# Kernel tuning notes

Hardware: AMD Instinct MI355X
Metric: run time of the kernel (lower is better)

Reference implementation:

```python
import jax, jax.numpy as jnp
import numpy as np
from jax import lax

N = 16384       # input points
STRIDE = 4
M = N // STRIDE # sampled centers (single batch: n_o = [o[0]//stride])
NSAMPLE = 16
CIN = 64
COUT = 128
EPS = 1e-5      # BatchNorm1d default eps


def setup_inputs() -> dict:
    key = jax.random.key(0)
    k1, k2, k3, k4 = jax.random.split(key, 4)
    p = jax.random.normal(k1, (N, 3), dtype=jnp.float32)
    n = jax.random.normal(k2, (N, 3), dtype=jnp.float32)
    x = jax.random.normal(k3, (N, CIN), dtype=jnp.float32)
    o = jnp.array([N], dtype=jnp.int32)  # single point cloud
    W = jax.random.normal(k4, (COUT, 3 + CIN), dtype=jnp.float32) * 0.05
    gamma = jnp.ones((COUT,), dtype=jnp.float32)
    beta = jnp.zeros((COUT,), dtype=jnp.float32)
    return {"p": p, "n": n, "x": x, "o": o, "W": W, "gamma": gamma, "beta": beta}


def _fps(p, m):
    """Furthest point sampling (pointops.furthestsampling), single batch."""
    npts = p.shape[0]
    def step(carry, _):
        dists, last = carry
        d = jnp.sum((p - p[last]) ** 2, axis=-1)
        dists = jnp.minimum(dists, d)
        nxt = jnp.argmax(dists).astype(jnp.int32)
        return (dists, nxt), nxt
    first = jnp.int32(0)
    init = (jnp.full((npts,), 1e10, dtype=p.dtype), first)
    _, rest = lax.scan(step, init, None, length=m - 1)
    return jnp.concatenate([first[None], rest])  # [m]


def reference(p, n, x, o, W, gamma, beta):
    # --- furthest sampling: n_o = [o[0]//stride] = [M] (static for single batch)
    idx = _fps(p, M)                      # [M] int32
    n_p = p[idx]                          # [M,3] new coords
    n_n = n[idx]                          # [M,3] new normals
    # --- queryandgroup: kNN of each center in full cloud, use_xyz=True
    d2 = (jnp.sum(n_p * n_p, -1)[:, None]
          + jnp.sum(p * p, -1)[None, :]
          - 2.0 * n_p @ p.T)              # [M,N]
    _, knn = lax.top_k(-lax.stop_gradient(d2), NSAMPLE)   # [M,NSAMPLE]
    grouped_xyz = p[knn] - n_p[:, None, :]                # [M,NS,3] relative coords
    grouped_x = x[knn]                                    # [M,NS,CIN]
    feat = jnp.concatenate([grouped_xyz, grouped_x], axis=-1)  # [M,NS,3+CIN]
    # --- linear (no bias) -> BN (training stats, per channel) -> ReLU -> max over neighbors
    y = jnp.einsum('msc,oc->mso', feat, W)                # [M,NS,COUT]
    mean = jnp.mean(y, axis=(0, 1))
    var = jnp.mean((y - mean) ** 2, axis=(0, 1))          # biased var (torch BN)
    y = (y - mean) * lax.rsqrt(var + EPS) * gamma + beta
    y = jax.nn.relu(y)
    y = jnp.max(y, axis=1)                                # MaxPool1d(nsample) -> [M,COUT]
    n_o = jnp.array([M], dtype=jnp.int32)
    return (n_p, n_n, y, n_o)
```

## Files before the change

kernel.cpp:

```cpp
#include <hip/hip_runtime.h>
#include <math.h>

#define N_PTS 16384
#define M_CTR 4096
#define NS 16
#define CIN 64
#define COUT 128
#define CFEAT 67
#define CPB 4
#define NCELL 512

__device__ __forceinline__ unsigned ordu(float f) {
    unsigned b = __float_as_uint(f);
    return (b & 0x80000000u) ? ~b : (b | 0x80000000u);
}
__device__ __forceinline__ float unord(unsigned u) {
    unsigned b = (u & 0x80000000u) ? (u & 0x7FFFFFFFu) : ~u;
    return __uint_as_float(b);
}

__device__ __forceinline__ void pmerge(unsigned long long& a1, unsigned long long& a2,
                                       unsigned long long b1, unsigned long long b2) {
    unsigned long long n1 = a1 > b1 ? a1 : b1;
    unsigned long long lo = a1 > b1 ? b1 : a1;
    unsigned long long m2 = a2 > b2 ? a2 : b2;
    a2 = lo > m2 ? lo : m2;
    a1 = n1;
}

#define DPP_TOP2(CTRL) do { \
    unsigned _o1lo = (unsigned)__builtin_amdgcn_update_dpp(0, (int)(unsigned)k1, CTRL, 0xF, 0xF, false); \
    unsigned _o1hi = (unsigned)__builtin_amdgcn_update_dpp(0, (int)(unsigned)(k1>>32), CTRL, 0xF, 0xF, false); \
    unsigned _o2lo = (unsigned)__builtin_amdgcn_update_dpp(0, (int)(unsigned)k2, CTRL, 0xF, 0xF, false); \
    unsigned _o2hi = (unsigned)__builtin_amdgcn_update_dpp(0, (int)(unsigned)(k2>>32), CTRL, 0xF, 0xF, false); \
    unsigned long long _b1 = ((unsigned long long)_o1hi << 32) | (unsigned long long)_o1lo; \
    unsigned long long _b2 = ((unsigned long long)_o2hi << 32) | (unsigned long long)_o2lo; \
    pmerge(k1, k2, _b1, _b2); \
} while (0)

#define DPP_SWEEP(M) M(0x111); M(0x112); M(0x114); M(0x118); M(0x142); M(0x143)

__global__ void init_kernel(unsigned* __restrict__ bmin, unsigned* __restrict__ bmax,
                            int* __restrict__ cnt, int* __restrict__ fill)
{
    int i = blockIdx.x * blockDim.x + threadIdx.x;
    if (i < NCELL * 3) { bmin[i] = 0xFFFFFFFFu; bmax[i] = 0u; }
    if (i < NCELL) { cnt[i] = 0; fill[i] = 0; }
}

__global__ __launch_bounds__(256) void bbox_kernel(const float* __restrict__ p,
                                                   float* __restrict__ gbb)
{
    int t = threadIdx.x, lane = t & 63, w = t >> 6;
    float mnx = 1e30f, mny = 1e30f, mnz = 1e30f;
    float mxx = -1e30f, mxy = -1e30f, mxz = -1e30f;
    for (int i = t; i < N_PTS; i += 256) {
        float x = p[i*3], y = p[i*3+1], z = p[i*3+2];
        mnx = fminf(mnx, x); mny = fminf(mny, y); mnz = fminf(mnz, z);
        mxx = fmaxf(mxx, x); mxy = fmaxf(mxy, y); mxz = fmaxf(mxz, z);
    }
    for (int m = 1; m < 64; m <<= 1) {
        mnx = fminf(mnx, __shfl_xor(mnx, m)); mny = fminf(mny, __shfl_xor(mny, m));
        mnz = fminf(mnz, __shfl_xor(mnz, m));
        mxx = fmaxf(mxx, __shfl_xor(mxx, m)); mxy = fmaxf(mxy, __shfl_xor(mxy, m));
        mxz = fmaxf(mxz, __shfl_xor(mxz, m));
    }
    __shared__ float s[4][6];
    if (lane == 0) { s[w][0]=mnx; s[w][1]=mny; s[w][2]=mnz; s[w][3]=mxx; s[w][4]=mxy; s[w][5]=mxz; }
    __syncthreads();
    if (t == 0) {
        gbb[0] = fminf(fminf(s[0][0], s[1][0]), fminf(s[2][0], s[3][0]));
        gbb[1] = fminf(fminf(s[0][1], s[1][1]), fminf(s[2][1], s[3][1]));
        gbb[2] = fminf(fminf(s[0][2], s[1][2]), fminf(s[2][2], s[3][2]));
        gbb[3] = fmaxf(fmaxf(s[0][3], s[1][3]), fmaxf(s[2][3], s[3][3]));
        gbb[4] = fmaxf(fmaxf(s[0][4], s[1][4]), fmaxf(s[2][4], s[3][4]));
        gbb[5] = fmaxf(fmaxf(s[0][5], s[1][5]), fmaxf(s[2][5], s[3][5]));
    }
}

__global__ void assign_kernel(const float* __restrict__ p, const float* __restrict__ gbb,
                              int* __restrict__ c_of, int* __restrict__ cnt)
{
    int i = blockIdx.x * blockDim.x + threadIdx.x;
    if (i >= N_PTS) return;
    float bx = gbb[0], by = gbb[1], bz = gbb[2];
    float sx = 7.9999f / fmaxf(gbb[3] - bx, 1e-20f);
    float sy = 7.9999f / fmaxf(gbb[4] - by, 1e-20f);
    float sz = 7.9999f / fmaxf(gbb[5] - bz, 1e-20f);
    float x = p[i*3], y = p[i*3+1], z = p[i*3+2];
    int ix = min(7, max(0, (int)((x - bx) * sx)));
    int iy = min(7, max(0, (int)((y - by) * sy)));
    int iz = min(7, max(0, (int)((z - bz) * sz)));
    int c = (ix << 6) | (iy << 3) | iz;
    c_of[i] = c;
    atomicAdd(&cnt[c], 1);
}

__global__ __launch_bounds__(512) void prefix_kernel(const int* __restrict__ cnt,
                                                     int* __restrict__ start,
                                                     int* __restrict__ cmeta)
{
    __shared__ int a[NCELL];
    int t = threadIdx.x;
    int v = cnt[t]; a[t] = v; __syncthreads();
    for (int off = 1; off < NCELL; off <<= 1) {
        int u = (t >= off) ? a[t - off] : 0;
        __syncthreads();
        a[t] += u;
        __syncthreads();
    }
    int st = a[t] - v;
    start[t] = st;
    cmeta[t] = (st << 15) | v;
}

__global__ void scatter_kernel(const float* __restrict__ p, const int* __restrict__ c_of,
                               const int* __restrict__ start, int* __restrict__ fill,
                               float4* __restrict__ sp, unsigned* __restrict__ bmin,
                               unsigned* __restrict__ bmax)
{
    int i = blockIdx.x * blockDim.x + threadIdx.x;
    if (i >= N_PTS) return;
    int c = c_of[i];
    int pos = start[c] + atomicAdd(&fill[c], 1);
    float x = p[i*3], y = p[i*3+1], z = p[i*3+2];
    sp[pos] = make_float4(x, y, z, __int_as_float(i));
    atomicMin(&bmin[c*3+0], ordu(x)); atomicMax(&bmax[c*3+0], ordu(x));
    atomicMin(&bmin[c*3+1], ordu(y)); atomicMax(&bmax[c*3+1], ordu(y));
    atomicMin(&bmin[c*3+2], ordu(z)); atomicMax(&bmax[c*3+2], ordu(z));
}

__global__ __launch_bounds__(1024) void fps_kernel(const float* __restrict__ p,
                                                   const float4* __restrict__ sp,
                                                   const int* __restrict__ g_cmeta,
                                                   const unsigned* __restrict__ g_bmin,
                                                   const unsigned* __restrict__ g_bmax,
                                                   int* __restrict__ sel)
{
    __shared__ float distl[N_PTS];
    __shared__ unsigned long long key1[NCELL], key2[NCELL];
    __shared__ int cmeta_s[NCELL];
    __shared__ unsigned short wl[NCELL];
    __shared__ float bq[6];
    __shared__ int bnsel;
    __shared__ int wlc;

    const int t = threadIdx.x;
    const int lane = t & 63, wave = t >> 6;

    for (int i = t; i < N_PTS; i += 1024) distl[i] = 1e10f;

    int my_cnt = 0;
    float mnx=0.f, mny=0.f, mnz=0.f, mxx=0.f, mxy=0.f, mxz=0.f;
    if (t < NCELL) {
        int meta = g_cmeta[t];
        cmeta_s[t] = meta;
        my_cnt = meta & 0x7FFF;
        mnx = unord(g_bmin[t*3+0]); mny = unord(g_bmin[t*3+1]); mnz = unord(g_bmin[t*3+2]);
        mxx = unord(g_bmax[t*3+0]); mxy = unord(g_bmax[t*3+1]); mxz = unord(g_bmax[t*3+2]);
        key1[t] = 0ull; key2[t] = 0ull;
    }
    if (t == 0) { wlc = 0; sel[0] = 0; }
    float q1x = p[0], q1y = p[1], q1z = p[2];
    float q2x = 0.f, q2y = 0.f, q2z = 0.f;
    bool two = false;
    bool first = true;
    __syncthreads();

    int it = 1;
    while (it < M_CTR) {
        bool act = false;
        if (my_cnt > 0) {
            if (first) act = true;
            else {
                float cm = __uint_as_float((unsigned)(key1[t] >> 32)) * 1.00001f;
                float ddx = fmaxf(fmaxf(__fsub_rn(mnx, q1x), __fsub_rn(q1x, mxx)), 0.f);
                float ddy = fmaxf(fmaxf(__fsub_rn(mny, q1y), __fsub_rn(q1y, mxy)), 0.f);
                float ddz = fmaxf(fmaxf(__fsub_rn(mnz, q1z), __fsub_rn(q1z, mxz)), 0.f);
                float dm1 = __fadd_rn(__fadd_rn(__fmul_rn(ddx,ddx), __fmul_rn(ddy,ddy)),
                                      __fmul_rn(ddz,ddz));
                act = dm1 < cm;
                if (!act && two) {
                    float ex = fmaxf(fmaxf(__fsub_rn(mnx, q2x), __fsub_rn(q2x, mxx)), 0.f);
                    float ey = fmaxf(fmaxf(__fsub_rn(mny, q2y), __fsub_rn(q2y, mxy)), 0.f);
                    float ez = fmaxf(fmaxf(__fsub_rn(mnz, q2z), __fsub_rn(q2z, mxz)), 0.f);
                    float dm2 = __fadd_rn(__fadd_rn(__fmul_rn(ex,ex), __fmul_rn(ey,ey)),
                                          __fmul_rn(ez,ez));
                    act = dm2 < cm;
                }
            }
        }
        unsigned long long mask = __ballot(act);
        int base = 0;
        if (lane == 0 && mask) base = atomicAdd(&wlc, (int)__popcll(mask));
        base = __shfl(base, 0);
        if (act)
            wl[base + (int)__popcll(mask & ((1ull << lane) - 1ull))] = (unsigned short)t;
        __syncthreads();
        const int nwl = wlc;

        for (int e = wave; e < nwl; e += 16) {
            int c = wl[e];
            int mv = cmeta_s[c];
            int st = mv >> 15, cnt = mv & 0x7FFF;
            unsigned long long k1 = 0ull, k2 = 0ull;
            for (int o = lane; o < cnt; o += 64) {
                int g = st + o;
                float4 P = sp[g];
                float D = distl[g];
                float dx = __fsub_rn(P.x, q1x), dy = __fsub_rn(P.y, q1y), dz = __fsub_rn(P.z, q1z);
                float d2 = __fadd_rn(__fadd_rn(__fmul_rn(dx,dx), __fmul_rn(dy,dy)),
                                     __fmul_rn(dz,dz));
                float nd = fminf(D, d2);
                if (two) {
                    float ex = __fsub_rn(P.x, q2x), ey = __fsub_rn(P.y, q2y), ez = __fsub_rn(P.z, q2z);
                    float e2 = __fadd_rn(__fadd_rn(__fmul_rn(ex,ex), __fmul_rn(ey,ey)),
                                         __fmul_rn(ez,ez));
                    nd = fminf(nd, e2);
                }
                distl[g] = nd;
                unsigned long long kk = ((unsigned long long)__float_as_uint(nd) << 32)
                                      | (unsigned long long)(~(unsigned)__float_as_int(P.w));
                if (kk > k1) { k2 = k1; k1 = kk; }
                else if (kk > k2) { k2 = kk; }
            }
            DPP_SWEEP(DPP_TOP2);
            if (lane == 63) { key1[c] = k1; key2[c] = k2; }
        }
        if (t == 1023) wlc = 0;
        __syncthreads();

        if (wave == 0) {
            unsigned long long k1 = 0ull, k2 = 0ull;
#pragma unroll
            for (int j = 0; j < 8; ++j) {
                int c = lane + (j << 6);
                pmerge(k1, k2, key1[c], key2[c]);
            }
            DPP_SWEEP(DPP_TOP2);
            if (lane == 63) {
                unsigned long long A1 = k1, A2 = k2;
                int s1 = (int)(~(unsigned)(A1 & 0xFFFFFFFFull));
                int s2 = (int)(~(unsigned)(A2 & 0xFFFFFFFFull));
                sel[it] = s1;
                float nq1x = p[s1*3+0], nq1y = p[s1*3+1], nq1z = p[s1*3+2];
                float bx2 = p[s2*3+0], by2 = p[s2*3+1], bz2 = p[s2*3+2];
                int nsel = 1;
                if (A2 != 0ull && it + 1 < M_CTR) {
                    float dx = __fsub_rn(bx2, nq1x), dy = __fsub_rn(by2, nq1y), dz = __fsub_rn(bz2, nq1z);
                    float d2b = __fadd_rn(__fadd_rn(__fmul_rn(dx,dx), __fmul_rn(dy,dy)),
                                          __fmul_rn(dz,dz));
                    float db = __uint_as_float((unsigned)(A2 >> 32));
                    if (d2b >= db) { nsel = 2; sel[it + 1] = s2; }
                }
                bq[0] = nq1x; bq[1] = nq1y; bq[2] = nq1z;
                bq[3] = bx2;  bq[4] = by2;  bq[5] = bz2;
                bnsel = nsel;
            }
        }
        __syncthreads();
        int nsel = bnsel;
        q1x = bq[0]; q1y = bq[1]; q1z = bq[2];
        two = (nsel == 2);
        if (two) { q2x = bq[3]; q2y = bq[4]; q2z = bq[5]; }
        first = false;
        it += nsel;
    }
}

__global__ void prep_kernel(const float* __restrict__ p, const float* __restrict__ nrm,
                            const int* __restrict__ sel, float* __restrict__ pp2,
                            float* __restrict__ out)
{
    int i = blockIdx.x * blockDim.x + threadIdx.x;
    if (i < N_PTS) {
        float x = p[i*3], y = p[i*3+1], z = p[i*3+2];
        pp2[i] = __fadd_rn(__fadd_rn(__fmul_rn(x,x), __fmul_rn(y,y)), __fmul_rn(z,z));
    }
    if (i < M_CTR) {
        int j = sel[i];
        out[i*3+0] = p[j*3+0]; out[i*3+1] = p[j*3+1]; out[i*3+2] = p[j*3+2];
        out[12288 + i*3+0] = nrm[j*3+0];
        out[12288 + i*3+1] = nrm[j*3+1];
        out[12288 + i*3+2] = nrm[j*3+2];
    }
    if (i == 0) out[548864] = (float)M_CTR;
}

__global__ __launch_bounds__(256) void knn_kernel(const float* __restrict__ p,
                                                  const float* __restrict__ pp2,
                                                  const float* __restrict__ np ,
                                                  int* __restrict__ knn)
{
    const int lane = threadIdx.x & 63;
    const int wave = threadIdx.x >> 6;
    const int c = blockIdx.x * 4 + wave;

    float cx = np[c*3], cy = np[c*3+1], cz = np[c*3+2];
    float c2 = __fadd_rn(__fadd_rn(__fmul_rn(cx,cx), __fmul_rn(cy,cy)), __fmul_rn(cz,cz));

    float hd[16]; int hi[16];
#pragma unroll
    for (int k = 0; k < 16; ++k) { hd[k] = 1e30f; hi[k] = 0x7fffffff; }

    for (int t = 0; t < N_PTS/64; ++t) {
        int j = t*64 + lane;
        float px = p[j*3+0], py = p[j*3+1], pz = p[j*3+2];
        float dot = __fadd_rn(__fadd_rn(__fmul_rn(cx,px), __fmul_rn(cy,py)),
                              __fmul_rn(cz,pz));
        float d2  = __fsub_rn(__fadd_rn(c2, pp2[j]), __fmul_rn(2.0f, dot));
        if (d2 < hd[15]) {
#pragma unroll
            for (int k = 15; k >= 1; --k) {
                bool up   = d2 < hd[k-1];
                bool here = d2 < hd[k];
                hd[k] = up ? hd[k-1] : (here ? d2 : hd[k]);
                hi[k] = up ? hi[k-1] : (here ? j  : hi[k]);
            }
            if (d2 < hd[0]) { hd[0] = d2; hi[0] = j; }
        }
    }

    for (int r = 0; r < 16; ++r) {
        float wv = hd[0]; int wi = hi[0];
#pragma unroll
        for (int m = 1; m < 64; m <<= 1) {
            float ov = __shfl_xor(wv, m);
            int   oi = __shfl_xor(wi, m);
            bool b = (ov < wv) || (ov == wv && oi < wi);
            wv = b ? ov : wv; wi = b ? oi : wi;
        }
        if (hi[0] == wi) {
            knn[c*16 + r] = wi;
#pragma unroll
            for (int k = 0; k < 15; ++k) { hd[k] = hd[k+1]; hi[k] = hi[k+1]; }
            hd[15] = 1e30f; hi[15] = 0x7fffffff;
        }
    }
}

__global__ __launch_bounds__(128) void passA_kernel(const float* __restrict__ p,
                                                    const float* __restrict__ xf,
                                                    const float* __restrict__ W,
                                                    const int* __restrict__ knn,
                                                    const float* __restrict__ out ,
                                                    float* __restrict__ ymax,
                                                    float* __restrict__ ymin,
                                                    float* __restrict__ partials)
{
    __shared__ float Wt[CFEAT][COUT];
    __shared__ float ft[CPB][NS][CFEAT];
    __shared__ float bsum[CPB][COUT], bssq[CPB][COUT];

    const int t = threadIdx.x;
    const int mbase = blockIdx.x * CPB;

    for (int c = 0; c < CFEAT; ++c) Wt[c][t] = W[t*CFEAT + c];

    {
        int r = t >> 1, half = t & 1;
        int ci = r >> 4, s = r & 15;
        int m = mbase + ci;
        int nb = knn[m*NS + s];
        if (half == 0) {
            ft[ci][s][0] = __fsub_rn(p[nb*3+0], out[m*3+0]);
            ft[ci][s][1] = __fsub_rn(p[nb*3+1], out[m*3+1]);
            ft[ci][s][2] = __fsub_rn(p[nb*3+2], out[m*3+2]);
        }
        for (int c = half*32; c < half*32 + 32; ++c)
            ft[ci][s][3+c] = xf[nb*CIN + c];
    }
    __syncthreads();

    const int ci = t >> 5, l = t & 31;
    float acc[NS][4];
#pragma unroll
    for (int s = 0; s < NS; ++s) { acc[s][0]=0.f; acc[s][1]=0.f; acc[s][2]=0.f; acc[s][3]=0.f; }

    for (int c = 0; c < CFEAT; ++c) {
        float w0 = Wt[c][l], w1 = Wt[c][l+32], w2 = Wt[c][l+64], w3 = Wt[c][l+96];
#pragma unroll
        for (int s = 0; s < NS; ++s) {
            float f = ft[ci][s][c];
            acc[s][0] = fmaf(f, w0, acc[s][0]);
            acc[s][1] = fmaf(f, w1, acc[s][1]);
            acc[s][2] = fmaf(f, w2, acc[s][2]);
            acc[s][3] = fmaf(f, w3, acc[s][3]);
        }
    }

    const int m = mbase + ci;
#pragma unroll
    for (int j = 0; j < 4; ++j) {
        int o = l + 32*j;
        float s = 0.f, q = 0.f, mx = -1e30f, mn = 1e30f;
#pragma unroll
        for (int sidx = 0; sidx < NS; ++sidx) {
            float v = acc[sidx][j];
            s += v; q = fmaf(v, v, q);
            mx = fmaxf(mx, v); mn = fminf(mn, v);
        }
        bsum[ci][o] = s;
        bssq[ci][o] = q;
        ymax[m*COUT + o] = mx;
        ymin[m*COUT + o] = mn;
    }
    __syncthreads();
    if (t < COUT) {
        float s = bsum[0][t] + bsum[1][t] + bsum[2][t] + bsum[3][t];
        float q = bssq[0][t] + bssq[1][t] + bssq[2][t] + bssq[3][t];
        partials[t*1024          + blockIdx.x] = s;
        partials[(COUT + t)*1024 + blockIdx.x] = q;
    }
}

__global__ __launch_bounds__(256) void bnstat_kernel(const float* __restrict__ partials,
                                                     const float* __restrict__ gamma,
                                                     const float* __restrict__ beta,
                                                     float* __restrict__ scaleshift)
{
    __shared__ float red[256];
    int t = threadIdx.x;
    const float4* v4 = (const float4*)(partials + t*1024);
    float s = 0.f;
    for (int i = 0; i < 256; ++i) {
        float4 v = v4[i];
        s += v.x; s += v.y; s += v.z; s += v.w;
    }
    red[t] = s;
    __syncthreads();
    if (t < COUT) {
        const float inv = 1.0f / 65536.0f;
        float mean = red[t] * inv;
        float var  = red[COUT + t] * inv - mean*mean;
        float rstd = rsqrtf(var + 1e-5f);
        float g = gamma[t] * rstd;
        scaleshift[t]        = g;
        scaleshift[COUT + t] = beta[t] - mean * g;
    }
}

__global__ void final_kernel(float* __restrict__ y,
                             const float* __restrict__ ymin,
                             const float* __restrict__ scaleshift)
{
    int i = blockIdx.x * blockDim.x + threadIdx.x;
    if (i >= M_CTR * COUT) return;
    int o = i & (COUT - 1);
    float a = scaleshift[o], b = scaleshift[COUT + o];
    float v = (a >= 0.f) ? y[i] : ymin[i];
    float z = fmaf(a, v, b);
    y[i] = fmaxf(z, 0.f);
}

extern "C" void kernel_launch(void* const* d_in, const int* in_sizes, int n_in,
                              void* d_out, int out_size, void* d_ws, size_t ws_size,
                              hipStream_t stream)
{
    const float* p     = (const float*)d_in[0];
    const float* nrm   = (const float*)d_in[1];
    const float* xf    = (const float*)d_in[2];
    const float* W     = (const float*)d_in[4];
    const float* gamma = (const float*)d_in[5];
    const float* beta  = (const float*)d_in[6];

    float* out = (float*)d_out;
    char* ws = (char*)d_ws;
    int*   sel        = (int*)(ws + 0);
    float* pp2        = (float*)(ws + 16384);
    int*   knn        = (int*)(ws + 81920);
    float* ymin       = (float*)(ws + 344064);
    float* partials   = (float*)(ws + 2441216);
    float* scaleshift = (float*)(ws + 3489792);

    float4*   sp        = (float4*)(ws + 81920);
    char*     yb        = ws + 344064;
    int*      c_of      = (int*)(yb + 65536);
    int*      cellcnt   = (int*)(yb + 131072);
    int*      cellfill  = (int*)(yb + 133120);
    int*      cellstart = (int*)(yb + 135168);
    unsigned* bbmin_u   = (unsigned*)(yb + 137216);
    unsigned* bbmax_u   = (unsigned*)(yb + 143360);
    float*    gbb       = (float*)(yb + 149504);
    int*      cmeta_g   = (int*)(yb + 149536);

    float* ymax = out + 24576;

    init_kernel   <<<8,  256, 0, stream>>>(bbmin_u, bbmax_u, cellcnt, cellfill);
    bbox_kernel   <<<1,  256, 0, stream>>>(p, gbb);
    assign_kernel <<<64, 256, 0, stream>>>(p, gbb, c_of, cellcnt);
    prefix_kernel <<<1,  512, 0, stream>>>(cellcnt, cellstart, cmeta_g);
    scatter_kernel<<<64, 256, 0, stream>>>(p, c_of, cellstart, cellfill, sp, bbmin_u, bbmax_u);
    fps_kernel    <<<1,  1024, 0, stream>>>(p, sp, cmeta_g, bbmin_u, bbmax_u, sel);
    prep_kernel   <<<64, 256, 0, stream>>>(p, nrm, sel, pp2, out);
    knn_kernel    <<<1024, 256, 0, stream>>>(p, pp2, out, knn);
    passA_kernel  <<<M_CTR/CPB, 128, 0, stream>>>(p, xf, W, knn, out, ymax, ymin, partials);
    bnstat_kernel <<<1, 256, 0, stream>>>(partials, gamma, beta, scaleshift);
    final_kernel  <<<2048, 256, 0, stream>>>(ymax, ymin, scaleshift);
}
```

Baseline: 6.438 ms.

## Keep FPS distances in registers with fixed 16-point per-thread chunks

New measurement: 6.698 ms. 1.04x slower.

```diff
diff --git a/kernel.cpp b/kernel.cpp
--- a/kernel.cpp
+++ b/kernel.cpp
@@ -8,16 +8,8 @@
 #define COUT 128
 #define CFEAT 67
 #define CPB 4
-#define NCELL 512
-
-__device__ __forceinline__ unsigned ordu(float f) {
-    unsigned b = __float_as_uint(f);
-    return (b & 0x80000000u) ? ~b : (b | 0x80000000u);
-}
-__device__ __forceinline__ float unord(unsigned u) {
-    unsigned b = (u & 0x80000000u) ? (u & 0x7FFFFFFFu) : ~u;
-    return __uint_as_float(b);
-}
+#define NCELL 4096
+#define PPT 16
 
 __device__ __forceinline__ void pmerge(unsigned long long& a1, unsigned long long& a2,
                                        unsigned long long b1, unsigned long long b2) {
@@ -40,11 +32,12 @@
 
 #define DPP_SWEEP(M) M(0x111); M(0x112); M(0x114); M(0x118); M(0x142); M(0x143)
 
-__global__ void init_kernel(unsigned* __restrict__ bmin, unsigned* __restrict__ bmax,
-                            int* __restrict__ cnt, int* __restrict__ fill)
+#define REPEAT16(M) M(0) M(1) M(2) M(3) M(4) M(5) M(6) M(7) \
+                    M(8) M(9) M(10) M(11) M(12) M(13) M(14) M(15)
+
+__global__ void init_kernel(int* __restrict__ cnt, int* __restrict__ fill)
 {
     int i = blockIdx.x * blockDim.x + threadIdx.x;
-    if (i < NCELL * 3) { bmin[i] = 0xFFFFFFFFu; bmax[i] = 0u; }
     if (i < NCELL) { cnt[i] = 0; fill[i] = 0; }
 }
 
@@ -84,159 +77,139 @@
     int i = blockIdx.x * blockDim.x + threadIdx.x;
     if (i >= N_PTS) return;
     float bx = gbb[0], by = gbb[1], bz = gbb[2];
-    float sx = 7.9999f / fmaxf(gbb[3] - bx, 1e-20f);
-    float sy = 7.9999f / fmaxf(gbb[4] - by, 1e-20f);
-    float sz = 7.9999f / fmaxf(gbb[5] - bz, 1e-20f);
+    float sx = 15.9999f / fmaxf(gbb[3] - bx, 1e-20f);
+    float sy = 15.9999f / fmaxf(gbb[4] - by, 1e-20f);
+    float sz = 15.9999f / fmaxf(gbb[5] - bz, 1e-20f);
     float x = p[i*3], y = p[i*3+1], z = p[i*3+2];
-    int ix = min(7, max(0, (int)((x - bx) * sx)));
-    int iy = min(7, max(0, (int)((y - by) * sy)));
-    int iz = min(7, max(0, (int)((z - bz) * sz)));
-    int c = (ix << 6) | (iy << 3) | iz;
+    int ix = min(15, max(0, (int)((x - bx) * sx)));
+    int iy = min(15, max(0, (int)((y - by) * sy)));
+    int iz = min(15, max(0, (int)((z - bz) * sz)));
+    int c = (ix << 8) | (iy << 4) | iz;
     c_of[i] = c;
     atomicAdd(&cnt[c], 1);
 }
 
-__global__ __launch_bounds__(512) void prefix_kernel(const int* __restrict__ cnt,
-                                                     int* __restrict__ start,
-                                                     int* __restrict__ cmeta)
-{
-    __shared__ int a[NCELL];
+__global__ __launch_bounds__(1024) void prefix_kernel(const int* __restrict__ cnt,
+                                                      int* __restrict__ start)
+{
+    __shared__ int a[1024];
     int t = threadIdx.x;
-    int v = cnt[t]; a[t] = v; __syncthreads();
-    for (int off = 1; off < NCELL; off <<= 1) {
+    int c0 = cnt[4*t], c1 = cnt[4*t+1], c2 = cnt[4*t+2], c3 = cnt[4*t+3];
+    int s = c0 + c1 + c2 + c3;
+    a[t] = s; __syncthreads();
+    for (int off = 1; off < 1024; off <<= 1) {
         int u = (t >= off) ? a[t - off] : 0;
         __syncthreads();
         a[t] += u;
         __syncthreads();
     }
-    int st = a[t] - v;
-    start[t] = st;
-    cmeta[t] = (st << 15) | v;
+    int ex = a[t] - s;
+    start[4*t]   = ex;
+    start[4*t+1] = ex + c0;
+    start[4*t+2] = ex + c0 + c1;
+    start[4*t+3] = ex + c0 + c1 + c2;
 }
 
 __global__ void scatter_kernel(const float* __restrict__ p, const int* __restrict__ c_of,
                                const int* __restrict__ start, int* __restrict__ fill,
-                               float4* __restrict__ sp, unsigned* __restrict__ bmin,
-                               unsigned* __restrict__ bmax)
+                               float4* __restrict__ sp)
 {
     int i = blockIdx.x * blockDim.x + threadIdx.x;
     if (i >= N_PTS) return;
     int c = c_of[i];
     int pos = start[c] + atomicAdd(&fill[c], 1);
-    float x = p[i*3], y = p[i*3+1], z = p[i*3+2];
-    sp[pos] = make_float4(x, y, z, __int_as_float(i));
-    atomicMin(&bmin[c*3+0], ordu(x)); atomicMax(&bmax[c*3+0], ordu(x));
-    atomicMin(&bmin[c*3+1], ordu(y)); atomicMax(&bmax[c*3+1], ordu(y));
-    atomicMin(&bmin[c*3+2], ordu(z)); atomicMax(&bmax[c*3+2], ordu(z));
+    sp[pos] = make_float4(p[i*3], p[i*3+1], p[i*3+2], __int_as_float(i));
 }
 
 __global__ __launch_bounds__(1024) void fps_kernel(const float* __restrict__ p,
                                                    const float4* __restrict__ sp,
-                                                   const int* __restrict__ g_cmeta,
-                                                   const unsigned* __restrict__ g_bmin,
-                                                   const unsigned* __restrict__ g_bmax,
                                                    int* __restrict__ sel)
 {
-    __shared__ float distl[N_PTS];
-    __shared__ unsigned long long key1[NCELL], key2[NCELL];
-    __shared__ int cmeta_s[NCELL];
-    __shared__ unsigned short wl[NCELL];
+    __shared__ unsigned long long skw1[16], skw2[16];
     __shared__ float bq[6];
     __shared__ int bnsel;
-    __shared__ int wlc;
 
     const int t = threadIdx.x;
     const int lane = t & 63, wave = t >> 6;
-
-    for (int i = t; i < N_PTS; i += 1024) distl[i] = 1e10f;
-
-    int my_cnt = 0;
-    float mnx=0.f, mny=0.f, mnz=0.f, mxx=0.f, mxy=0.f, mxz=0.f;
-    if (t < NCELL) {
-        int meta = g_cmeta[t];
-        cmeta_s[t] = meta;
-        my_cnt = meta & 0x7FFF;
-        mnx = unord(g_bmin[t*3+0]); mny = unord(g_bmin[t*3+1]); mnz = unord(g_bmin[t*3+2]);
-        mxx = unord(g_bmax[t*3+0]); mxy = unord(g_bmax[t*3+1]); mxz = unord(g_bmax[t*3+2]);
-        key1[t] = 0ull; key2[t] = 0ull;
-    }
-    if (t == 0) { wlc = 0; sel[0] = 0; }
+    const int base = t << 4;
+
+#define DECL(k) float ds##k = 1e10f;
+    REPEAT16(DECL)
+#undef DECL
+
+    float bmnx = 1e30f, bmny = 1e30f, bmnz = 1e30f;
+    float bmxx = -1e30f, bmxy = -1e30f, bmxz = -1e30f;
+#define BBX(k) { float4 P = sp[base + k]; \
+    bmnx = fminf(bmnx, P.x); bmny = fminf(bmny, P.y); bmnz = fminf(bmnz, P.z); \
+    bmxx = fmaxf(bmxx, P.x); bmxy = fmaxf(bmxy, P.y); bmxz = fmaxf(bmxz, P.z); }
+    REPEAT16(BBX)
+#undef BBX
+
+    float tmax = 1e10f;
+    unsigned long long kc1 = 0ull, kc2 = 0ull;
+
+    if (t == 0) sel[0] = 0;
     float q1x = p[0], q1y = p[1], q1z = p[2];
     float q2x = 0.f, q2y = 0.f, q2z = 0.f;
-    bool two = false;
-    bool first = true;
+    bool two = false, first = true;
     __syncthreads();
 
     int it = 1;
     while (it < M_CTR) {
-        bool act = false;
-        if (my_cnt > 0) {
-            if (first) act = true;
-            else {
-                float cm = __uint_as_float((unsigned)(key1[t] >> 32)) * 1.00001f;
-                float ddx = fmaxf(fmaxf(__fsub_rn(mnx, q1x), __fsub_rn(q1x, mxx)), 0.f);
-                float ddy = fmaxf(fmaxf(__fsub_rn(mny, q1y), __fsub_rn(q1y, mxy)), 0.f);
-                float ddz = fmaxf(fmaxf(__fsub_rn(mnz, q1z), __fsub_rn(q1z, mxz)), 0.f);
-                float dm1 = __fadd_rn(__fadd_rn(__fmul_rn(ddx,ddx), __fmul_rn(ddy,ddy)),
-                                      __fmul_rn(ddz,ddz));
-                act = dm1 < cm;
-                if (!act && two) {
-                    float ex = fmaxf(fmaxf(__fsub_rn(mnx, q2x), __fsub_rn(q2x, mxx)), 0.f);
-                    float ey = fmaxf(fmaxf(__fsub_rn(mny, q2y), __fsub_rn(q2y, mxy)), 0.f);
-                    float ez = fmaxf(fmaxf(__fsub_rn(mnz, q2z), __fsub_rn(q2z, mxz)), 0.f);
-                    float dm2 = __fadd_rn(__fadd_rn(__fmul_rn(ex,ex), __fmul_rn(ey,ey)),
-                                          __fmul_rn(ez,ez));
-                    act = dm2 < cm;
-                }
+        bool act;
+        if (first) act = true;
+        else {
+            float cm = tmax * 1.00001f;
+            float ddx = fmaxf(fmaxf(__fsub_rn(bmnx, q1x), __fsub_rn(q1x, bmxx)), 0.f);
+            float ddy = fmaxf(fmaxf(__fsub_rn(bmny, q1y), __fsub_rn(q1y, bmxy)), 0.f);
+            float ddz = fmaxf(fmaxf(__fsub_rn(bmnz, q1z), __fsub_rn(q1z, bmxz)), 0.f);
+            float dm1 = __fadd_rn(__fadd_rn(__fmul_rn(ddx,ddx), __fmul_rn(ddy,ddy)),
+                                  __fmul_rn(ddz,ddz));
+            act = dm1 < cm;
+            if (!act && two) {
+                float ex = fmaxf(fmaxf(__fsub_rn(bmnx, q2x), __fsub_rn(q2x, bmxx)), 0.f);
+                float ey = fmaxf(fmaxf(__fsub_rn(bmny, q2y), __fsub_rn(q2y, bmxy)), 0.f);
+                float ez = fmaxf(fmaxf(__fsub_rn(bmnz, q2z), __fsub_rn(q2z, bmxz)), 0.f);
+                float dm2 = __fadd_rn(__fadd_rn(__fmul_rn(ex,ex), __fmul_rn(ey,ey)),
+                                      __fmul_rn(ez,ez));
+                act = dm2 < cm;
             }
         }
-        unsigned long long mask = __ballot(act);
-        int base = 0;
-        if (lane == 0 && mask) base = atomicAdd(&wlc, (int)__popcll(mask));
-        base = __shfl(base, 0);
-        if (act)
-            wl[base + (int)__popcll(mask & ((1ull << lane) - 1ull))] = (unsigned short)t;
+
+        if (act) {
+            float nmax = -1.0f;
+            unsigned long long k1 = 0ull, k2 = 0ull;
+#define UPD(k) { \
+            float4 P = sp[base + k]; \
+            float dx = __fsub_rn(P.x, q1x), dy = __fsub_rn(P.y, q1y), dz = __fsub_rn(P.z, q1z); \
+            float d2 = __fadd_rn(__fadd_rn(__fmul_rn(dx,dx), __fmul_rn(dy,dy)), \
+                                 __fmul_rn(dz,dz)); \
+            float nd = fminf(ds##k, d2); \
+            if (two) { \
+                float ex = __fsub_rn(P.x, q2x), ey = __fsub_rn(P.y, q2y), ez = __fsub_rn(P.z, q2z); \
+                float e2 = __fadd_rn(__fadd_rn(__fmul_rn(ex,ex), __fmul_rn(ey,ey)), \
+                                     __fmul_rn(ez,ez)); \
+                nd = fminf(nd, e2); \
+            } \
+            ds##k = nd; \
+            nmax = fmaxf(nmax, nd); \
+            unsigned long long kk = ((unsigned long long)__float_as_uint(nd) << 32) \
+                                  | (unsigned long long)(~(unsigned)__float_as_int(P.w)); \
+            if (kk > k1) { k2 = k1; k1 = kk; } else if (kk > k2) { k2 = kk; } }
+            REPEAT16(UPD)
+#undef UPD
+            tmax = nmax;
+            kc1 = k1; kc2 = k2;
+        }
+
+        unsigned long long k1 = kc1, k2 = kc2;
+        DPP_SWEEP(DPP_TOP2);
+        if (lane == 63) { skw1[wave] = k1; skw2[wave] = k2; }
         __syncthreads();
-        const int nwl = wlc;
-
-        for (int e = wave; e < nwl; e += 16) {
-            int c = wl[e];
-            int mv = cmeta_s[c];
-            int st = mv >> 15, cnt = mv & 0x7FFF;
-            unsigned long long k1 = 0ull, k2 = 0ull;
-            for (int o = lane; o < cnt; o += 64) {
-                int g = st + o;
-                float4 P = sp[g];
-                float D = distl[g];
-                float dx = __fsub_rn(P.x, q1x), dy = __fsub_rn(P.y, q1y), dz = __fsub_rn(P.z, q1z);
-                float d2 = __fadd_rn(__fadd_rn(__fmul_rn(dx,dx), __fmul_rn(dy,dy)),
-                                     __fmul_rn(dz,dz));
-                float nd = fminf(D, d2);
-                if (two) {
-                    float ex = __fsub_rn(P.x, q2x), ey = __fsub_rn(P.y, q2y), ez = __fsub_rn(P.z, q2z);
-                    float e2 = __fadd_rn(__fadd_rn(__fmul_rn(ex,ex), __fmul_rn(ey,ey)),
-                                         __fmul_rn(ez,ez));
-                    nd = fminf(nd, e2);
-                }
-                distl[g] = nd;
-                unsigned long long kk = ((unsigned long long)__float_as_uint(nd) << 32)
-                                      | (unsigned long long)(~(unsigned)__float_as_int(P.w));
-                if (kk > k1) { k2 = k1; k1 = kk; }
-                else if (kk > k2) { k2 = kk; }
-            }
-            DPP_SWEEP(DPP_TOP2);
-            if (lane == 63) { key1[c] = k1; key2[c] = k2; }
-        }
-        if (t == 1023) wlc = 0;
-        __syncthreads();
 
         if (wave == 0) {
-            unsigned long long k1 = 0ull, k2 = 0ull;
-#pragma unroll
-            for (int j = 0; j < 8; ++j) {
-                int c = lane + (j << 6);
-                pmerge(k1, k2, key1[c], key2[c]);
-            }
+            k1 = (lane < 16) ? skw1[lane] : 0ull;
+            k2 = (lane < 16) ? skw2[lane] : 0ull;
             DPP_SWEEP(DPP_TOP2);
             if (lane == 63) {
                 unsigned long long A1 = k1, A2 = k2;
@@ -477,21 +450,18 @@
     char*     yb        = ws + 344064;
     int*      c_of      = (int*)(yb + 65536);
     int*      cellcnt   = (int*)(yb + 131072);
-    int*      cellfill  = (int*)(yb + 133120);
-    int*      cellstart = (int*)(yb + 135168);
-    unsigned* bbmin_u   = (unsigned*)(yb + 137216);
-    unsigned* bbmax_u   = (unsigned*)(yb + 143360);
-    float*    gbb       = (float*)(yb + 149504);
-    int*      cmeta_g   = (int*)(yb + 149536);
+    int*      cellfill  = (int*)(yb + 147456);
+    int*      cellstart = (int*)(yb + 163840);
+    float*    gbb       = (float*)(yb + 180224);
 
     float* ymax = out + 24576;
 
-    init_kernel   <<<8,  256, 0, stream>>>(bbmin_u, bbmax_u, cellcnt, cellfill);
+    init_kernel   <<<16, 256, 0, stream>>>(cellcnt, cellfill);
     bbox_kernel   <<<1,  256, 0, stream>>>(p, gbb);
     assign_kernel <<<64, 256, 0, stream>>>(p, gbb, c_of, cellcnt);
-    prefix_kernel <<<1,  512, 0, stream>>>(cellcnt, cellstart, cmeta_g);
-    scatter_kernel<<<64, 256, 0, stream>>>(p, c_of, cellstart, cellfill, sp, bbmin_u, bbmax_u);
-    fps_kernel    <<<1,  1024, 0, stream>>>(p, sp, cmeta_g, bbmin_u, bbmax_u, sel);
+    prefix_kernel <<<1,  1024, 0, stream>>>(cellcnt, cellstart);
+    scatter_kernel<<<64, 256, 0, stream>>>(p, c_of, cellstart, cellfill, sp);
+    fps_kernel    <<<1,  1024, 0, stream>>>(p, sp, sel);
     prep_kernel   <<<64, 256, 0, stream>>>(p, nrm, sel, pp2, out);
     knn_kernel    <<<1024, 256, 0, stream>>>(p, pp2, out, knn);
     passA_kernel  <<<M_CTR/CPB, 128, 0, stream>>>(p, xf, W, knn, out, ymax, ymin, partials);
```
